# Kernel optimization log

Measured on AMD Instinct MI355X. Metric: run time of the kernel, lower is better.

## Reference

```python
import jax, jax.numpy as jnp
import numpy as np

D_MODEL = 128; D_STATE = 64; HEADDIM = 32; D_CONV = 4; EXPAND = 2
D_INNER = EXPAND * D_MODEL          # 256
NHEADS = D_INNER // HEADDIM         # 8
NGROUPS = 1
D_CONV_CH = D_INNER + 2 * NGROUPS * D_STATE      # 384
D_IN_PROJ = 2 * D_INNER + 2 * NGROUPS * D_STATE + NHEADS  # 648


def _mamba2(u, Win, convw, convb, dtb, Alog, Dp, normw, Wout):
    # u: (B, L, d_model). Mamba2 forward (ngroups=1, rmsnorm gated, no in/out bias).
    B, L, _ = u.shape
    zxbcdt = u @ Win                                   # (B,L,648)
    z, xBC, dt = jnp.split(zxbcdt, [D_INNER, D_INNER + D_CONV_CH], axis=-1)
    # depthwise causal conv1d (kernel D_CONV) + SiLU
    xp = jnp.pad(xBC, ((0, 0), (D_CONV - 1, 0), (0, 0)))
    xconv = sum(xp[:, k:k + L, :] * convw[k] for k in range(D_CONV)) + convb
    xBC = jax.nn.silu(xconv)
    x, Bm, Cm = jnp.split(xBC, [D_INNER, D_INNER + NGROUPS * D_STATE], axis=-1)
    dt = jax.nn.softplus(dt + dtb)                     # (B,L,H)
    A = -jnp.exp(Alog)                                 # (H,)
    xh = x.reshape(B, L, NHEADS, HEADDIM)              # (B,L,H,P)
    dA = jnp.exp(dt * A)                               # (B,L,H)

    def step(h, inp):
        dA_t, dt_t, B_t, C_t, x_t = inp
        h = h * dA_t[:, :, None, None] + jnp.einsum('bh,bn,bhp->bhpn', dt_t, B_t, x_t)
        y = jnp.einsum('bhpn,bn->bhp', h, C_t)
        return h, y

    h0 = jnp.zeros((B, NHEADS, HEADDIM, D_STATE), dtype=u.dtype)
    xs = (jnp.moveaxis(dA, 1, 0), jnp.moveaxis(dt, 1, 0), jnp.moveaxis(Bm, 1, 0),
          jnp.moveaxis(Cm, 1, 0), jnp.moveaxis(xh, 1, 0))
    _, ys = jax.lax.scan(step, h0, xs)
    y = jnp.moveaxis(ys, 0, 1) + Dp[None, None, :, None] * xh   # skip D
    y = y.reshape(B, L, D_INNER)
    # RMSNormGated (norm_before_gate=False): rmsnorm(y * silu(z)) * weight
    y = y * jax.nn.silu(z)
    y = y * jax.lax.rsqrt(jnp.mean(y * y, axis=-1, keepdims=True) + 1e-5) * normw
    return y @ Wout


def _cross_attn(x, ctx, Wq, bq, Wk, bk, Wv, bv, Wo, bo):
    Q = x @ Wq + bq
    K = ctx @ Wk + bk
    V = ctx @ Wv + bv
    att = jax.nn.softmax(jnp.einsum('bqd,bkd->bqk', Q, K) * (D_MODEL ** -0.5), axis=-1)
    return jnp.einsum('bqk,bkd->bqd', att, V) @ Wo + bo


def setup_inputs() -> dict:
    key = jax.random.key(0)
    ks = jax.random.split(key, 8)
    B, L = 2048, 8

    def lin(k, fi, fo):
        return jax.random.normal(k, (fi, fo), jnp.float32) / np.sqrt(fi)

    def mamba_params(kseq):
        k = jax.random.split(kseq, 6)
        dt = jax.random.uniform(k[3], (NHEADS,), minval=0.001, maxval=0.1)
        return {
            'Win': lin(k[0], D_MODEL, D_IN_PROJ),
            'convw': jax.random.normal(k[1], (D_CONV, D_CONV_CH), jnp.float32) * 0.2,
            'convb': jnp.zeros((D_CONV_CH,), jnp.float32),
            'dtb': dt + jnp.log(-jnp.expm1(-dt)),  # inverse softplus
            'Alog': jnp.log(jax.random.uniform(k[4], (NHEADS,), minval=1.0, maxval=16.0)),
            'D': jnp.ones((NHEADS,), jnp.float32),
            'normw': jnp.ones((D_INNER,), jnp.float32),
            'Wout': lin(k[5], D_INNER, D_MODEL),
        }

    inp = {
        'st_feature': jax.random.normal(ks[0], (B, L, D_MODEL), jnp.float32),
        'exp_feature': jax.random.normal(ks[1], (B, L, D_MODEL), jnp.float32),
    }
    for pref, p in (('st_', mamba_params(ks[2])), ('ex_', mamba_params(ks[3]))):
        for n, v in p.items():
            inp[pref + n] = v

    def ca(kseq, pref):
        k = jax.random.split(kseq, 4)
        d = {}
        for n, kk in zip(('Wq', 'Wk', 'Wv', 'Wo'), k):
            d[pref + n] = lin(kk, D_MODEL, D_MODEL)
            d[pref + 'b' + n[1]] = jnp.zeros((D_MODEL,), jnp.float32)
        return d

    inp.update(ca(ks[4], 'cx_'))  # cross_atten_exp
    inp.update(ca(ks[5], 'cs_'))  # cross_atten_st
    inp['mlp_W'] = lin(ks[6], 8 * 2 * D_MODEL, 1024)
    inp['mlp_b'] = jnp.zeros((1024,), jnp.float32)
    return inp


def reference(st_feature, exp_feature,
              st_Win, st_convw, st_convb, st_dtb, st_Alog, st_D, st_normw, st_Wout,
              ex_Win, ex_convw, ex_convb, ex_dtb, ex_Alog, ex_D, ex_normw, ex_Wout,
              cx_Wq, cx_bq, cx_Wk, cx_bk, cx_Wv, cx_bv, cx_Wo, cx_bo,
              cs_Wq, cs_bq, cs_Wk, cs_bk, cs_Wv, cs_bv, cs_Wo, cs_bo,
              mlp_W, mlp_b):
    exp_f = _mamba2(exp_feature, ex_Win, ex_convw, ex_convb, ex_dtb, ex_Alog, ex_D, ex_normw, ex_Wout)
    st_f = _mamba2(st_feature, st_Win, st_convw, st_convb, st_dtb, st_Alog, st_D, st_normw, st_Wout)
    exp_a = _cross_attn(exp_f, st_f, cx_Wq, cx_bq, cx_Wk, cx_bk, cx_Wv, cx_bv, cx_Wo, cx_bo)
    st_a = _cross_attn(st_f, exp_f, cs_Wq, cs_bq, cs_Wk, cs_bk, cs_Wv, cs_bv, cs_Wo, cs_bo)
    x = jnp.concatenate([st_a, exp_a], axis=-1)        # (B, 8, 256)
    x = x.reshape(x.shape[0], -1)                      # (B, 2048)
    return x @ mlp_W + mlp_b
```

## Files before the change

kernel.cpp:

```cpp
#include <hip/hip_runtime.h>
#include <hip/hip_bf16.h>
#include <math.h>

#define B_SZ 2048
#define L_SEQ 8
#define DMODEL 128
#define DSTATE 64
#define HEADDIM 32
#define DCONV 4
#define DINNER 256
#define NHEADS 8
#define DCONVCH 384
#define DINPROJ 648
#define NPAD 656

typedef short bf16x8 __attribute__((ext_vector_type(8)));
typedef float floatx4 __attribute__((ext_vector_type(4)));

__device__ __forceinline__ float siluf(float x) {
    return x / (1.f + expf(-x));
}
__device__ __forceinline__ float bf2f(unsigned short h) {
    unsigned int u = ((unsigned int)h) << 16;
    return __builtin_bit_cast(float, u);
}
__device__ __forceinline__ unsigned short f2bf(float f) {
    __hip_bfloat16 b = __float2bfloat16(f);
    return __builtin_bit_cast(unsigned short, b);
}
__device__ __forceinline__ void unpack8(bf16x8 v, float* o) {
    #pragma unroll
    for (int j = 0; j < 8; ++j) o[j] = bf2f((unsigned short)v[j]);
}
__device__ __forceinline__ void gl_lds16(const unsigned short* g, unsigned short* l) {
    __builtin_amdgcn_global_load_lds(
        (const __attribute__((address_space(1))) unsigned int*)g,
        (__attribute__((address_space(3))) unsigned int*)l, 16, 0, 0);
}

__global__ __launch_bounds__(256) void prep_weights(
    const float* __restrict__ st_Win, const float* __restrict__ ex_Win,
    const float* __restrict__ st_Wout, const float* __restrict__ ex_Wout,
    const float* __restrict__ cs_Wq, const float* __restrict__ cs_Wk,
    const float* __restrict__ cs_Wv, const float* __restrict__ cs_Wo,
    const float* __restrict__ cx_Wq, const float* __restrict__ cx_Wk,
    const float* __restrict__ cx_Wv, const float* __restrict__ cx_Wo,
    const float* __restrict__ mlp_W,
    unsigned short* __restrict__ winT_st, unsigned short* __restrict__ winT_ex,
    unsigned short* __restrict__ woutT_st, unsigned short* __restrict__ woutT_ex,
    unsigned short* __restrict__ attnWT, unsigned short* __restrict__ mlpWt)
{
    __shared__ float tile[32][33];
    int blk = blockIdx.x;
    if (blk < 656) {
        const float* src = blk < 328 ? st_Win : ex_Win;
        unsigned short* dst = blk < 328 ? winT_st : winT_ex;
        int idx = (blk % 328) * 256 + threadIdx.x;
        if (idx >= NPAD * 128) return;
        int n = idx / 128, k = idx % 128;
        float v = (n < DINPROJ) ? src[k * DINPROJ + n] : 0.f;
        dst[idx] = f2bf(v);
    } else if (blk < 912) {
        const float* src = blk < 784 ? st_Wout : ex_Wout;
        unsigned short* dst = blk < 784 ? woutT_st : woutT_ex;
        int idx = ((blk - 656) % 128) * 256 + threadIdx.x;
        int n = idx / 256, k = idx % 256;
        dst[idx] = f2bf(src[k * 128 + n]);
    } else if (blk < 1424) {
        int b2 = blk - 912;
        int mat = b2 >> 6;
        const float* src = mat == 0 ? cs_Wq : mat == 1 ? cs_Wk : mat == 2 ? cs_Wv :
                           mat == 3 ? cs_Wo : mat == 4 ? cx_Wq : mat == 5 ? cx_Wk :
                           mat == 6 ? cx_Wv : cx_Wo;
        int e = (b2 & 63) * 256 + threadIdx.x;
        int n = e >> 7, k = e & 127;
        attnWT[mat * 16384 + n * 128 + k] = f2bf(src[k * 128 + n]);
    } else {
        int b2 = blk - 1424;
        int n0 = (b2 & 31) * 32, k0 = (b2 >> 5) * 32;
        const int tid = threadIdx.x;
        const int c = tid & 31, r0 = tid >> 5;
        for (int rr = r0; rr < 32; rr += 8)
            tile[rr][c] = mlp_W[(size_t)(k0 + rr) * 1024 + n0 + c];
        __syncthreads();
        for (int rr = r0; rr < 32; rr += 8)
            mlpWt[(size_t)(n0 + rr) * 2048 + k0 + c] = f2bf(tile[c][rr]);
    }
}

#define LDK 136
#define LDZ 648
#define LDY 264
__global__ __launch_bounds__(256, 4) void mamba_dual(
    const float* __restrict__ u_ex, const float* __restrict__ u_st,
    const unsigned short* __restrict__ WinT_ex, const unsigned short* __restrict__ WinT_st,
    const float* __restrict__ convw_ex, const float* __restrict__ convw_st,
    const float* __restrict__ convb_ex, const float* __restrict__ convb_st,
    const float* __restrict__ dtb_ex, const float* __restrict__ dtb_st,
    const float* __restrict__ Alog_ex, const float* __restrict__ Alog_st,
    const float* __restrict__ Dp_ex, const float* __restrict__ Dp_st,
    const float* __restrict__ normw_ex, const float* __restrict__ normw_st,
    const unsigned short* __restrict__ WoutT_ex, const unsigned short* __restrict__ WoutT_st,
    unsigned short* __restrict__ out_ex, unsigned short* __restrict__ out_st)
{
    const int which = blockIdx.x >> 10;
    const float* u = which ? u_st : u_ex;
    const unsigned short* WinT = which ? WinT_st : WinT_ex;
    const float* convw = which ? convw_st : convw_ex;
    const float* convb = which ? convb_st : convb_ex;
    const float* dtb = which ? dtb_st : dtb_ex;
    const float* Alog = which ? Alog_st : Alog_ex;
    const float* Dp = which ? Dp_st : Dp_ex;
    const float* normw = which ? normw_st : normw_ex;
    const unsigned short* WoutT = which ? WoutT_st : WoutT_ex;
    unsigned short* outf = which ? out_st : out_ex;

    const int tid = threadIdx.x;
    const int lane = tid & 63;
    const int wave = tid >> 6;
    const int l15 = lane & 15;
    const int q8 = (lane >> 4) * 8;
    const int row0 = (lane >> 4) * 4;
    const int grow0 = (blockIdx.x & 1023) * 16;

    __shared__ __align__(16) unsigned short uA[16 * LDK];
    __shared__ __align__(16) unsigned short zx[16 * LDZ];
    __shared__ __align__(16) unsigned short yb[16 * LDY];
    __shared__ float dtraw[16][8];
    __shared__ float dtv[2][8][8];
    __shared__ float cum[2][8][8];
    __shared__ float Gm[2][8][8];
    __shared__ float red[16][32];
    __shared__ float rstd[16];
    float* coefp = (float*)uA;

    for (int i = tid; i < 512; i += 256) {
        int r = i >> 5, k4 = (i & 31) * 4;
        float4 v = *(const float4*)(u + (size_t)(grow0 + r) * DMODEL + k4);
        ushort4 h;
        h.x = f2bf(v.x); h.y = f2bf(v.y); h.z = f2bf(v.z); h.w = f2bf(v.w);
        *(ushort4*)(uA + r * LDK + k4) = h;
    }
    __syncthreads();

    {
        bf16x8 af[4];
        #pragma unroll
        for (int kk = 0; kk < 4; ++kk)
            af[kk] = *(const bf16x8*)(uA + l15 * LDK + kk * 32 + q8);
        for (int nt = wave; nt < 41; nt += 4) {
            floatx4 acc = {0.f, 0.f, 0.f, 0.f};
            const unsigned short* bp = WinT + (size_t)(nt * 16 + l15) * 128 + q8;
            #pragma unroll
            for (int kk = 0; kk < 4; ++kk) {
                bf16x8 bf = *(const bf16x8*)(bp + kk * 32);
                acc = __builtin_amdgcn_mfma_f32_16x16x32_bf16(af[kk], bf, acc, 0, 0, 0);
            }
            if (nt == 40) {
                if (l15 < 8) {
                    #pragma unroll
                    for (int r = 0; r < 4; ++r)
                        dtraw[row0 + r][l15] = acc[r];
                }
            } else {
                #pragma unroll
                for (int r = 0; r < 4; ++r)
                    zx[(row0 + r) * LDZ + nt * 16 + l15] = f2bf(acc[r]);
            }
        }
    }
    __syncthreads();

    float cv[3][8];
    {
        #pragma unroll
        for (int it = 0; it < 3; ++it) {
            int i = tid + it * 256;
            int r = i / 48, g = i % 48;
            int c0 = g * 8;
            int l = r & 7, bloc = r >> 3;
            float s[8];
            float4 cb0 = *(const float4*)(convb + c0);
            float4 cb1 = *(const float4*)(convb + c0 + 4);
            s[0] = cb0.x; s[1] = cb0.y; s[2] = cb0.z; s[3] = cb0.w;
            s[4] = cb1.x; s[5] = cb1.y; s[6] = cb1.z; s[7] = cb1.w;
            #pragma unroll
            for (int k = 0; k < DCONV; ++k) {
                int lp = l + k - (DCONV - 1);
                if (lp >= 0) {
                    bf16x8 v = *(const bf16x8*)(zx + (bloc * 8 + lp) * LDZ + 256 + c0);
                    float vf[8];
                    unpack8(v, vf);
                    float4 w0 = *(const float4*)(convw + k * DCONVCH + c0);
                    float4 w1 = *(const float4*)(convw + k * DCONVCH + c0 + 4);
                    s[0] += vf[0] * w0.x; s[1] += vf[1] * w0.y;
                    s[2] += vf[2] * w0.z; s[3] += vf[3] * w0.w;
                    s[4] += vf[4] * w1.x; s[5] += vf[5] * w1.y;
                    s[6] += vf[6] * w1.z; s[7] += vf[7] * w1.w;
                }
            }
            #pragma unroll
            for (int j = 0; j < 8; ++j) cv[it][j] = siluf(s[j]);
        }
        if (tid < 128) {
            int r = tid >> 3, h = tid & 7;
            float v = dtraw[r][h] + dtb[h];
            dtv[r >> 3][r & 7][h] = (v > 20.f) ? v : log1pf(expf(v));
        }
    }
    __syncthreads();
    {
        #pragma unroll
        for (int it = 0; it < 3; ++it) {
            int i = tid + it * 256;
            int r = i / 48, c0 = (i % 48) * 8;
            bf16x8 o;
            #pragma unroll
            for (int j = 0; j < 8; ++j) o[j] = (short)f2bf(cv[it][j]);
            *(bf16x8*)(zx + r * LDZ + 256 + c0) = o;
        }
    }
    __syncthreads();

    if (tid < 128) {
        int bloc = tid >> 6, t = (tid >> 3) & 7, s = tid & 7;
        float a = 0.f;
        #pragma unroll
        for (int n = 0; n < DSTATE; n += 8) {
            bf16x8 bv = *(const bf16x8*)(zx + (bloc * 8 + s) * LDZ + 512 + n);
            bf16x8 cvv = *(const bf16x8*)(zx + (bloc * 8 + t) * LDZ + 576 + n);
            float bf_[8], cf_[8];
            unpack8(bv, bf_); unpack8(cvv, cf_);
            #pragma unroll
            for (int j = 0; j < 8; ++j) a += bf_[j] * cf_[j];
        }
        Gm[bloc][t][s] = a;
    } else if (tid < 144) {
        int j = tid - 128;
        int bloc = j >> 3, h = j & 7;
        float c = 0.f;
        for (int l = 0; l < L_SEQ; ++l) { c += dtv[bloc][l][h]; cum[bloc][l][h] = c; }
    }
    __syncthreads();

    for (int i = tid; i < 1024; i += 256) {
        int bloc = i >> 9, t = (i >> 6) & 7, s = (i >> 3) & 7, h = i & 7;
        float A = -expf(Alog[h]);
        coefp[i] = (s <= t)
            ? Gm[bloc][t][s] * expf(A * (cum[bloc][t][h] - cum[bloc][s][h])) * dtv[bloc][s][h]
            : 0.f;
    }
    __syncthreads();

    {
        #pragma unroll
        for (int it = 0; it < 2; ++it) {
            int i = tid + it * 256;
            int r = i >> 5, g = i & 31;
            int c0 = g * 8, h = g >> 2;
            int bloc = r >> 3, t = r & 7;
            float acc[8];
            {
                bf16x8 xv = *(const bf16x8*)(zx + r * LDZ + 256 + c0);
                float xf[8]; unpack8(xv, xf);
                float d = Dp[h];
                #pragma unroll
                for (int j = 0; j < 8; ++j) acc[j] = d * xf[j];
            }
            for (int s = 0; s <= t; ++s) {
                float cf = coefp[((bloc * 8 + t) * 8 + s) * 8 + h];
                bf16x8 xv = *(const bf16x8*)(zx + (bloc * 8 + s) * LDZ + 256 + c0);
                float xf[8]; unpack8(xv, xf);
                #pragma unroll
                for (int j = 0; j < 8; ++j) acc[j] += cf * xf[j];
            }
            bf16x8 zv = *(const bf16x8*)(zx + r * LDZ + c0);
            float zf[8]; unpack8(zv, zf);
            float p = 0.f;
            bf16x8 o;
            #pragma unroll
            for (int j = 0; j < 8; ++j) {
                float y = acc[j] * siluf(zf[j]);
                p += y * y;
                o[j] = (short)f2bf(y);
            }
            *(bf16x8*)(yb + r * LDY + c0) = o;
            red[r][g] = p;
        }
    }
    __syncthreads();
    if (tid < 16) {
        float s = 0.f;
        #pragma unroll
        for (int j = 0; j < 32; ++j) s += red[tid][j];
        rstd[tid] = rsqrtf(s / (float)DINNER + 1e-5f);
    }
    __syncthreads();
    {
        #pragma unroll
        for (int it = 0; it < 2; ++it) {
            int i = tid + it * 256;
            int r = i >> 5, c0 = (i & 31) * 8;
            bf16x8 v = *(const bf16x8*)(yb + r * LDY + c0);
            float vf[8]; unpack8(v, vf);
            float4 w0 = *(const float4*)(normw + c0);
            float4 w1 = *(const float4*)(normw + c0 + 4);
            float rs = rstd[r];
            bf16x8 o;
            o[0] = (short)f2bf(vf[0] * rs * w0.x); o[1] = (short)f2bf(vf[1] * rs * w0.y);
            o[2] = (short)f2bf(vf[2] * rs * w0.z); o[3] = (short)f2bf(vf[3] * rs * w0.w);
            o[4] = (short)f2bf(vf[4] * rs * w1.x); o[5] = (short)f2bf(vf[5] * rs * w1.y);
            o[6] = (short)f2bf(vf[6] * rs * w1.z); o[7] = (short)f2bf(vf[7] * rs * w1.w);
            *(bf16x8*)(yb + r * LDY + c0) = o;
        }
    }
    __syncthreads();

    {
        bf16x8 af[8];
        #pragma unroll
        for (int kk = 0; kk < 8; ++kk)
            af[kk] = *(const bf16x8*)(yb + l15 * LDY + kk * 32 + q8);
        #pragma unroll
        for (int ni = 0; ni < 2; ++ni) {
            int nt = wave * 2 + ni;
            floatx4 acc = {0.f, 0.f, 0.f, 0.f};
            const unsigned short* bp = WoutT + (size_t)(nt * 16 + l15) * 256 + q8;
            #pragma unroll
            for (int kk = 0; kk < 8; ++kk) {
                bf16x8 bf = *(const bf16x8*)(bp + kk * 32);
                acc = __builtin_amdgcn_mfma_f32_16x16x32_bf16(af[kk], bf, acc, 0, 0, 0);
            }
            #pragma unroll
            for (int r = 0; r < 4; ++r)
                outf[(size_t)(grow0 + row0 + r) * DMODEL + nt * 16 + l15] = f2bf(acc[r]);
        }
    }
}

#define ASTR 136
#define VSTR 40
#define PSTR 40
__global__ __launch_bounds__(256, 2) void attn_kernel(
    const unsigned short* __restrict__ st_f,
    const unsigned short* __restrict__ exp_f,
    const unsigned short* __restrict__ WT,
    const float* __restrict__ cs_bq, const float* __restrict__ cs_bk,
    const float* __restrict__ cs_bv, const float* __restrict__ cs_bo,
    const float* __restrict__ cx_bq, const float* __restrict__ cx_bk,
    const float* __restrict__ cx_bv, const float* __restrict__ cx_bo,
    __hip_bfloat16* __restrict__ x)
{
    const int tid = threadIdx.x;
    const int lane = tid & 63, wave = tid >> 6;
    const int l15 = lane & 15;
    const int q8 = (lane >> 4) * 8;
    const int row0 = (lane >> 4) * 4;
    const int grow0 = blockIdx.x * 32;
    const int b0 = blockIdx.x * 4;
    const float scale = 0.08838834764831845f;

    __shared__ __align__(16) unsigned short stf[32 * ASTR];
    __shared__ __align__(16) unsigned short exf[32 * ASTR];
    __shared__ __align__(16) unsigned short Qs[32 * ASTR];
    __shared__ __align__(16) unsigned short Ks[32 * ASTR];
    __shared__ __align__(16) unsigned short attv[32 * ASTR];
    __shared__ __align__(16) unsigned short Vt[128 * VSTR];
    __shared__ __align__(16) unsigned short P[32 * PSTR];
    __shared__ float Ss[32][33];

    #pragma unroll
    for (int it = 0; it < 2; ++it) {
        int i = tid + it * 256;
        int r = i >> 4, c8 = (i & 15) * 8;
        *(uint4*)(stf + r * ASTR + c8) = *(const uint4*)(st_f + (size_t)(grow0 + r) * 128 + c8);
        *(uint4*)(exf + r * ASTR + c8) = *(const uint4*)(exp_f + (size_t)(grow0 + r) * 128 + c8);
    }
    __syncthreads();

    #pragma unroll
    for (int pass = 0; pass < 2; ++pass) {
        const unsigned short* qsrc = pass ? exf : stf;
        const unsigned short* kvsrc = pass ? stf : exf;
        const unsigned short* Wq = WT + (size_t)pass * 4 * 16384;
        const unsigned short* Wk = Wq + 16384;
        const unsigned short* Wv = Wq + 32768;
        const unsigned short* Wo = Wq + 49152;
        const float* bq = pass ? cx_bq : cs_bq;
        const float* bk = pass ? cx_bk : cs_bk;
        const float* bv = pass ? cx_bv : cs_bv;
        const float* bo = pass ? cx_bo : cs_bo;

        {
            bf16x8 aq[2][4], akv[2][4];
            #pragma unroll
            for (int mt = 0; mt < 2; ++mt)
                #pragma unroll
                for (int kk = 0; kk < 4; ++kk) {
                    aq[mt][kk]  = *(const bf16x8*)(qsrc  + (mt * 16 + l15) * ASTR + kk * 32 + q8);
                    akv[mt][kk] = *(const bf16x8*)(kvsrc + (mt * 16 + l15) * ASTR + kk * 32 + q8);
                }
            #pragma unroll
            for (int ni = 0; ni < 2; ++ni) {
                int nc = (wave * 2 + ni) * 16 + l15;
                floatx4 aq0 = {0,0,0,0}, aq1 = {0,0,0,0};
                floatx4 ak0 = {0,0,0,0}, ak1 = {0,0,0,0};
                floatx4 av0 = {0,0,0,0}, av1 = {0,0,0,0};
                #pragma unroll
                for (int kk = 0; kk < 4; ++kk) {
                    bf16x8 wqf = *(const bf16x8*)(Wq + (size_t)nc * 128 + kk * 32 + q8);
                    bf16x8 wkf = *(const bf16x8*)(Wk + (size_t)nc * 128 + kk * 32 + q8);
                    bf16x8 wvf = *(const bf16x8*)(Wv + (size_t)nc * 128 + kk * 32 + q8);
                    aq0 = __builtin_amdgcn_mfma_f32_16x16x32_bf16(aq[0][kk],  wqf, aq0, 0, 0, 0);
                    aq1 = __builtin_amdgcn_mfma_f32_16x16x32_bf16(aq[1][kk],  wqf, aq1, 0, 0, 0);
                    ak0 = __builtin_amdgcn_mfma_f32_16x16x32_bf16(akv[0][kk], wkf, ak0, 0, 0, 0);
                    ak1 = __builtin_amdgcn_mfma_f32_16x16x32_bf16(akv[1][kk], wkf, ak1, 0, 0, 0);
                    av0 = __builtin_amdgcn_mfma_f32_16x16x32_bf16(akv[0][kk], wvf, av0, 0, 0, 0);
                    av1 = __builtin_amdgcn_mfma_f32_16x16x32_bf16(akv[1][kk], wvf, av1, 0, 0, 0);
                }
                float bqv = bq[nc], bkv = bk[nc], bvv = bv[nc];
                #pragma unroll
                for (int r = 0; r < 4; ++r) {
                    Qs[(row0 + r) * ASTR + nc]      = f2bf(aq0[r] + bqv);
                    Qs[(16 + row0 + r) * ASTR + nc] = f2bf(aq1[r] + bqv);
                    Ks[(row0 + r) * ASTR + nc]      = f2bf(ak0[r] + bkv);
                    Ks[(16 + row0 + r) * ASTR + nc] = f2bf(ak1[r] + bkv);
                    Vt[nc * VSTR + row0 + r]        = f2bf(av0[r] + bvv);
                    Vt[nc * VSTR + 16 + row0 + r]   = f2bf(av1[r] + bvv);
                }
            }
        }
        __syncthreads();

        {
            int mtS = wave >> 1, ntS = wave & 1;
            floatx4 s = {0,0,0,0};
            #pragma unroll
            for (int kk = 0; kk < 4; ++kk) {
                bf16x8 a = *(const bf16x8*)(Qs + (mtS * 16 + l15) * ASTR + kk * 32 + q8);
                bf16x8 b = *(const bf16x8*)(Ks + (ntS * 16 + l15) * ASTR + kk * 32 + q8);
                s = __builtin_amdgcn_mfma_f32_16x16x32_bf16(a, b, s, 0, 0, 0);
            }
            #pragma unroll
            for (int r = 0; r < 4; ++r)
                Ss[mtS * 16 + row0 + r][ntS * 16 + l15] = s[r];
        }
        __syncthreads();

        if (tid < 32) {
            int r = tid, c0 = (r >> 3) * 8;
            float v[8], mx = -1e30f;
            #pragma unroll
            for (int c = 0; c < 8; ++c) {
                v[c] = Ss[r][c0 + c] * scale;
                mx = fmaxf(mx, v[c]);
            }
            float sum = 0.f;
            #pragma unroll
            for (int c = 0; c < 8; ++c) { v[c] = expf(v[c] - mx); sum += v[c]; }
            float inv = 1.f / sum;
            #pragma unroll
            for (int c = 0; c < 32; ++c) {
                float pv = (c >= c0 && c < c0 + 8) ? v[c - c0] * inv : 0.f;
                P[r * PSTR + c] = f2bf(pv);
            }
        }
        __syncthreads();

        {
            #pragma unroll
            for (int ni = 0; ni < 2; ++ni) {
                int nc = (wave * 2 + ni) * 16 + l15;
                bf16x8 bv_ = *(const bf16x8*)(Vt + nc * VSTR + q8);
                #pragma unroll
                for (int mt = 0; mt < 2; ++mt) {
                    bf16x8 ap = *(const bf16x8*)(P + (mt * 16 + l15) * PSTR + q8);
                    floatx4 o = {0,0,0,0};
                    o = __builtin_amdgcn_mfma_f32_16x16x32_bf16(ap, bv_, o, 0, 0, 0);
                    #pragma unroll
                    for (int r = 0; r < 4; ++r)
                        attv[(mt * 16 + row0 + r) * ASTR + nc] = f2bf(o[r]);
                }
            }
        }
        __syncthreads();

        {
            bf16x8 ao[2][4];
            #pragma unroll
            for (int mt = 0; mt < 2; ++mt)
                #pragma unroll
                for (int kk = 0; kk < 4; ++kk)
                    ao[mt][kk] = *(const bf16x8*)(attv + (mt * 16 + l15) * ASTR + kk * 32 + q8);
            #pragma unroll
            for (int ni = 0; ni < 2; ++ni) {
                int nc = (wave * 2 + ni) * 16 + l15;
                floatx4 a0 = {0,0,0,0}, a1 = {0,0,0,0};
                #pragma unroll
                for (int kk = 0; kk < 4; ++kk) {
                    bf16x8 wof = *(const bf16x8*)(Wo + (size_t)nc * 128 + kk * 32 + q8);
                    a0 = __builtin_amdgcn_mfma_f32_16x16x32_bf16(ao[0][kk], wof, a0, 0, 0, 0);
                    a1 = __builtin_amdgcn_mfma_f32_16x16x32_bf16(ao[1][kk], wof, a1, 0, 0, 0);
                }
                float bov = bo[nc];
                #pragma unroll
                for (int r = 0; r < 4; ++r) {
                    int rr0 = row0 + r;
                    int rr1 = 16 + row0 + r;
                    x[(size_t)(b0 + (rr0 >> 3)) * 2048 + (rr0 & 7) * 256 + pass * 128 + nc] =
                        __float2bfloat16(a0[r] + bov);
                    x[(size_t)(b0 + (rr1 >> 3)) * 2048 + (rr1 & 7) * 256 + pass * 128 + nc] =
                        __float2bfloat16(a1[r] + bov);
                }
            }
        }
        __syncthreads();
    }
}

__global__ __launch_bounds__(256, 2) void mlp_mfma(
    const unsigned short* __restrict__ X,
    const unsigned short* __restrict__ Wt,
    const float* __restrict__ bias,
    float* __restrict__ out)
{
    __shared__ __align__(16) unsigned short As[64 * 64];
    __shared__ __align__(16) unsigned short Bs[64 * 64];
    const int tid = threadIdx.x;
    const int wave = tid >> 6, lane = tid & 63;
    const int wm = (wave >> 1) * 32, wn = (wave & 1) * 32;
    const int bm = blockIdx.y * 64, bn = blockIdx.x * 64;
    const int l15 = lane & 15, q8 = (lane >> 4) * 8;

    const int c0i = tid, c1i = tid + 256;
    const int r0s = c0i >> 3, c0s = ((c0i & 7) ^ (r0s & 7)) * 8;
    const int r1s = c1i >> 3, c1s = ((c1i & 7) ^ (r1s & 7)) * 8;
    const unsigned short* gA0 = X + (size_t)(bm + r0s) * 2048 + c0s;
    const unsigned short* gA1 = X + (size_t)(bm + r1s) * 2048 + c1s;
    const unsigned short* gB0 = Wt + (size_t)(bn + r0s) * 2048 + c0s;
    const unsigned short* gB1 = Wt + (size_t)(bn + r1s) * 2048 + c1s;
    unsigned short* lA0 = As + c0i * 8;
    unsigned short* lA1 = As + c1i * 8;
    unsigned short* lB0 = Bs + c0i * 8;
    unsigned short* lB1 = Bs + c1i * 8;

    floatx4 acc[2][2];
    #pragma unroll
    for (int i = 0; i < 2; ++i)
        #pragma unroll
        for (int j = 0; j < 2; ++j) acc[i][j] = (floatx4){0.f, 0.f, 0.f, 0.f};

    const int ra0 = wm + l15, ra1 = wm + 16 + l15;
    const int rb0 = wn + l15, rb1 = wn + 16 + l15;

    for (int k0 = 0; k0 < 2048; k0 += 64) {
        __syncthreads();
        gl_lds16(gA0 + k0, lA0);
        gl_lds16(gA1 + k0, lA1);
        gl_lds16(gB0 + k0, lB0);
        gl_lds16(gB1 + k0, lB1);
        __syncthreads();
        #pragma unroll
        for (int ks = 0; ks < 2; ++ks) {
            int xx = ks * 4 + (q8 >> 3);
            bf16x8 a0 = *(const bf16x8*)(As + (ra0 * 8 + (xx ^ (ra0 & 7))) * 8);
            bf16x8 a1 = *(const bf16x8*)(As + (ra1 * 8 + (xx ^ (ra1 & 7))) * 8);
            bf16x8 b0 = *(const bf16x8*)(Bs + (rb0 * 8 + (xx ^ (rb0 & 7))) * 8);
            bf16x8 b1 = *(const bf16x8*)(Bs + (rb1 * 8 + (xx ^ (rb1 & 7))) * 8);
            acc[0][0] = __builtin_amdgcn_mfma_f32_16x16x32_bf16(a0, b0, acc[0][0], 0, 0, 0);
            acc[0][1] = __builtin_amdgcn_mfma_f32_16x16x32_bf16(a0, b1, acc[0][1], 0, 0, 0);
            acc[1][0] = __builtin_amdgcn_mfma_f32_16x16x32_bf16(a1, b0, acc[1][0], 0, 0, 0);
            acc[1][1] = __builtin_amdgcn_mfma_f32_16x16x32_bf16(a1, b1, acc[1][1], 0, 0, 0);
        }
    }

    const int row0 = (lane >> 4) * 4;
    #pragma unroll
    for (int j = 0; j < 2; ++j) {
        int col = bn + wn + j * 16 + l15;
        float bv = bias[col];
        #pragma unroll
        for (int r = 0; r < 4; ++r) {
            out[(size_t)(bm + wm + row0 + r) * 1024 + col] = acc[0][j][r] + bv;
            out[(size_t)(bm + wm + 16 + row0 + r) * 1024 + col] = acc[1][j][r] + bv;
        }
    }
}

extern "C" void kernel_launch(void* const* d_in, const int* in_sizes, int n_in,
                              void* d_out, int out_size, void* d_ws, size_t ws_size,
                              hipStream_t stream) {
    const float* st_feature = (const float*)d_in[0];
    const float* exp_feature = (const float*)d_in[1];
    const float* st_Win = (const float*)d_in[2];
    const float* st_convw = (const float*)d_in[3];
    const float* st_convb = (const float*)d_in[4];
    const float* st_dtb = (const float*)d_in[5];
    const float* st_Alog = (const float*)d_in[6];
    const float* st_D = (const float*)d_in[7];
    const float* st_normw = (const float*)d_in[8];
    const float* st_Wout = (const float*)d_in[9];
    const float* ex_Win = (const float*)d_in[10];
    const float* ex_convw = (const float*)d_in[11];
    const float* ex_convb = (const float*)d_in[12];
    const float* ex_dtb = (const float*)d_in[13];
    const float* ex_Alog = (const float*)d_in[14];
    const float* ex_D = (const float*)d_in[15];
    const float* ex_normw = (const float*)d_in[16];
    const float* ex_Wout = (const float*)d_in[17];
    const float* cx_Wq = (const float*)d_in[18]; const float* cx_bq = (const float*)d_in[19];
    const float* cx_Wk = (const float*)d_in[20]; const float* cx_bk = (const float*)d_in[21];
    const float* cx_Wv = (const float*)d_in[22]; const float* cx_bv = (const float*)d_in[23];
    const float* cx_Wo = (const float*)d_in[24]; const float* cx_bo = (const float*)d_in[25];
    const float* cs_Wq = (const float*)d_in[26]; const float* cs_bq = (const float*)d_in[27];
    const float* cs_Wk = (const float*)d_in[28]; const float* cs_bk = (const float*)d_in[29];
    const float* cs_Wv = (const float*)d_in[30]; const float* cs_bv = (const float*)d_in[31];
    const float* cs_Wo = (const float*)d_in[32]; const float* cs_bo = (const float*)d_in[33];
    const float* mlp_W = (const float*)d_in[34];
    const float* mlp_b = (const float*)d_in[35];

    unsigned short* wsu = (unsigned short*)d_ws;
    unsigned short* st_fb  = wsu;
    unsigned short* exp_fb = st_fb + (size_t)B_SZ * L_SEQ * DMODEL;
    unsigned short* xbuf   = exp_fb + (size_t)B_SZ * L_SEQ * DMODEL;
    unsigned short* wtbuf  = xbuf + (size_t)2048 * 2048;
    unsigned short* winT_st = wtbuf + (size_t)1024 * 2048;
    unsigned short* winT_ex = winT_st + (size_t)NPAD * 128;
    unsigned short* woutT_st = winT_ex + (size_t)NPAD * 128;
    unsigned short* woutT_ex = woutT_st + (size_t)128 * 256;
    unsigned short* attnWT  = woutT_ex + (size_t)128 * 256;

    prep_weights<<<3472, 256, 0, stream>>>(
        st_Win, ex_Win, st_Wout, ex_Wout,
        cs_Wq, cs_Wk, cs_Wv, cs_Wo, cx_Wq, cx_Wk, cx_Wv, cx_Wo, mlp_W,
        winT_st, winT_ex, woutT_st, woutT_ex, attnWT, wtbuf);
    mamba_dual<<<2048, 256, 0, stream>>>(
        exp_feature, st_feature, winT_ex, winT_st,
        ex_convw, st_convw, ex_convb, st_convb,
        ex_dtb, st_dtb, ex_Alog, st_Alog, ex_D, st_D,
        ex_normw, st_normw, woutT_ex, woutT_st,
        exp_fb, st_fb);
    attn_kernel<<<B_SZ / 4, 256, 0, stream>>>(st_fb, exp_fb, attnWT,
                                              cs_bq, cs_bk, cs_bv, cs_bo,
                                              cx_bq, cx_bk, cx_bv, cx_bo,
                                              (__hip_bfloat16*)xbuf);
    {
        dim3 g(1024 / 64, 2048 / 64);
        mlp_mfma<<<g, 256, 0, stream>>>(xbuf, wtbuf, mlp_b, (float*)d_out);
    }
}
```

Before: 253.5 us.

## Cut mamba LDS usage for occupancy and enlarge MLP GEMM tile to 128x64

The mamba kernel drops its separate y buffer and reduction array. It keeps gated y values in registers, computes the RMS sum with wave shuffles, and writes the normalized output into the reused zx buffer. This lets launch bounds rise to 5 blocks per CU. The MLP GEMM tile grows from 64x64 to 128x64 with 4x2 MFMA accumulators per wave, which improves A/B reuse and halves the grid. The tradeoffs are higher register pressure and fewer blocks in the MLP, and reusing zx as ybA assumes zx is no longer read when it is overwritten.

```diff
diff --git a/kernel.cpp b/kernel.cpp
--- a/kernel.cpp
+++ b/kernel.cpp
@@ -91,7 +91,7 @@
 #define LDK 136
 #define LDZ 648
 #define LDY 264
-__global__ __launch_bounds__(256, 4) void mamba_dual(
+__global__ __launch_bounds__(256, 5) void mamba_dual(
     const float* __restrict__ u_ex, const float* __restrict__ u_st,
     const unsigned short* __restrict__ WinT_ex, const unsigned short* __restrict__ WinT_st,
     const float* __restrict__ convw_ex, const float* __restrict__ convw_st,
@@ -125,14 +125,13 @@
 
     __shared__ __align__(16) unsigned short uA[16 * LDK];
     __shared__ __align__(16) unsigned short zx[16 * LDZ];
-    __shared__ __align__(16) unsigned short yb[16 * LDY];
     __shared__ float dtraw[16][8];
     __shared__ float dtv[2][8][8];
     __shared__ float cum[2][8][8];
     __shared__ float Gm[2][8][8];
-    __shared__ float red[16][32];
     __shared__ float rstd[16];
     float* coefp = (float*)uA;
+    unsigned short* ybA = zx;
 
     for (int i = tid; i < 512; i += 256) {
         int r = i >> 5, k4 = (i & 31) * 4;
@@ -252,7 +251,9 @@
     }
     __syncthreads();
 
+    float yv[2][8];
     {
+        float psum[2];
         #pragma unroll
         for (int it = 0; it < 2; ++it) {
             int i = tid + it * 256;
@@ -277,41 +278,45 @@
             bf16x8 zv = *(const bf16x8*)(zx + r * LDZ + c0);
             float zf[8]; unpack8(zv, zf);
             float p = 0.f;
-            bf16x8 o;
             #pragma unroll
             for (int j = 0; j < 8; ++j) {
                 float y = acc[j] * siluf(zf[j]);
                 p += y * y;
-                o[j] = (short)f2bf(y);
-            }
-            *(bf16x8*)(yb + r * LDY + c0) = o;
-            red[r][g] = p;
-        }
-    }
-    __syncthreads();
-    if (tid < 16) {
-        float s = 0.f;
-        #pragma unroll
-        for (int j = 0; j < 32; ++j) s += red[tid][j];
-        rstd[tid] = rsqrtf(s / (float)DINNER + 1e-5f);
-    }
-    __syncthreads();
+                yv[it][j] = y;
+            }
+            psum[it] = p;
+        }
+        #pragma unroll
+        for (int off = 16; off > 0; off >>= 1) {
+            psum[0] += __shfl_down(psum[0], off, 32);
+            psum[1] += __shfl_down(psum[1], off, 32);
+        }
+        if ((lane & 31) == 0) {
+            int r = tid >> 5;
+            rstd[r]     = rsqrtf(psum[0] * (1.f / DINNER) + 1e-5f);
+            rstd[r + 8] = rsqrtf(psum[1] * (1.f / DINNER) + 1e-5f);
+        }
+    }
+    __syncthreads();
+
     {
         #pragma unroll
         for (int it = 0; it < 2; ++it) {
             int i = tid + it * 256;
             int r = i >> 5, c0 = (i & 31) * 8;
-            bf16x8 v = *(const bf16x8*)(yb + r * LDY + c0);
-            float vf[8]; unpack8(v, vf);
+            float rs = rstd[r];
             float4 w0 = *(const float4*)(normw + c0);
             float4 w1 = *(const float4*)(normw + c0 + 4);
-            float rs = rstd[r];
             bf16x8 o;
-            o[0] = (short)f2bf(vf[0] * rs * w0.x); o[1] = (short)f2bf(vf[1] * rs * w0.y);
-            o[2] = (short)f2bf(vf[2] * rs * w0.z); o[3] = (short)f2bf(vf[3] * rs * w0.w);
-            o[4] = (short)f2bf(vf[4] * rs * w1.x); o[5] = (short)f2bf(vf[5] * rs * w1.y);
-            o[6] = (short)f2bf(vf[6] * rs * w1.z); o[7] = (short)f2bf(vf[7] * rs * w1.w);
-            *(bf16x8*)(yb + r * LDY + c0) = o;
+            o[0] = (short)f2bf(yv[it][0] * rs * w0.x);
+            o[1] = (short)f2bf(yv[it][1] * rs * w0.y);
+            o[2] = (short)f2bf(yv[it][2] * rs * w0.z);
+            o[3] = (short)f2bf(yv[it][3] * rs * w0.w);
+            o[4] = (short)f2bf(yv[it][4] * rs * w1.x);
+            o[5] = (short)f2bf(yv[it][5] * rs * w1.y);
+            o[6] = (short)f2bf(yv[it][6] * rs * w1.z);
+            o[7] = (short)f2bf(yv[it][7] * rs * w1.w);
+            *(bf16x8*)(ybA + r * LDY + c0) = o;
         }
     }
     __syncthreads();
@@ -320,7 +325,7 @@
         bf16x8 af[8];
         #pragma unroll
         for (int kk = 0; kk < 8; ++kk)
-            af[kk] = *(const bf16x8*)(yb + l15 * LDY + kk * 32 + q8);
+            af[kk] = *(const bf16x8*)(ybA + l15 * LDY + kk * 32 + q8);
         #pragma unroll
         for (int ni = 0; ni < 2; ++ni) {
             int nt = wave * 2 + ni;
@@ -518,71 +523,80 @@
     }
 }
 
-__global__ __launch_bounds__(256, 2) void mlp_mfma(
+__global__ __launch_bounds__(256) void mlp_mfma(
     const unsigned short* __restrict__ X,
     const unsigned short* __restrict__ Wt,
     const float* __restrict__ bias,
     float* __restrict__ out)
 {
-    __shared__ __align__(16) unsigned short As[64 * 64];
+    __shared__ __align__(16) unsigned short As[128 * 64];
     __shared__ __align__(16) unsigned short Bs[64 * 64];
     const int tid = threadIdx.x;
     const int wave = tid >> 6, lane = tid & 63;
-    const int wm = (wave >> 1) * 32, wn = (wave & 1) * 32;
-    const int bm = blockIdx.y * 64, bn = blockIdx.x * 64;
+    const int wm = (wave >> 1) * 64, wn = (wave & 1) * 32;
+    const int bm = blockIdx.y * 128, bn = blockIdx.x * 64;
     const int l15 = lane & 15, q8 = (lane >> 4) * 8;
 
-    const int c0i = tid, c1i = tid + 256;
-    const int r0s = c0i >> 3, c0s = ((c0i & 7) ^ (r0s & 7)) * 8;
-    const int r1s = c1i >> 3, c1s = ((c1i & 7) ^ (r1s & 7)) * 8;
-    const unsigned short* gA0 = X + (size_t)(bm + r0s) * 2048 + c0s;
-    const unsigned short* gA1 = X + (size_t)(bm + r1s) * 2048 + c1s;
-    const unsigned short* gB0 = Wt + (size_t)(bn + r0s) * 2048 + c0s;
-    const unsigned short* gB1 = Wt + (size_t)(bn + r1s) * 2048 + c1s;
-    unsigned short* lA0 = As + c0i * 8;
-    unsigned short* lA1 = As + c1i * 8;
-    unsigned short* lB0 = Bs + c0i * 8;
-    unsigned short* lB1 = Bs + c1i * 8;
-
-    floatx4 acc[2][2];
+    const unsigned short* gA[4];
+    const unsigned short* gB[2];
     #pragma unroll
-    for (int i = 0; i < 2; ++i)
+    for (int j = 0; j < 4; ++j) {
+        int cid = tid + j * 256;
+        int r = cid >> 3, c16 = ((cid & 7) ^ (r & 7)) * 8;
+        gA[j] = X + (size_t)(bm + r) * 2048 + c16;
+    }
+    #pragma unroll
+    for (int j = 0; j < 2; ++j) {
+        int cid = tid + j * 256;
+        int r = cid >> 3, c16 = ((cid & 7) ^ (r & 7)) * 8;
+        gB[j] = Wt + (size_t)(bn + r) * 2048 + c16;
+    }
+
+    floatx4 acc[4][2];
+    #pragma unroll
+    for (int i = 0; i < 4; ++i)
         #pragma unroll
         for (int j = 0; j < 2; ++j) acc[i][j] = (floatx4){0.f, 0.f, 0.f, 0.f};
 
-    const int ra0 = wm + l15, ra1 = wm + 16 + l15;
-    const int rb0 = wn + l15, rb1 = wn + 16 + l15;
-
     for (int k0 = 0; k0 < 2048; k0 += 64) {
         __syncthreads();
-        gl_lds16(gA0 + k0, lA0);
-        gl_lds16(gA1 + k0, lA1);
-        gl_lds16(gB0 + k0, lB0);
-        gl_lds16(gB1 + k0, lB1);
+        #pragma unroll
+        for (int j = 0; j < 4; ++j) gl_lds16(gA[j] + k0, As + (tid + j * 256) * 8);
+        #pragma unroll
+        for (int j = 0; j < 2; ++j) gl_lds16(gB[j] + k0, Bs + (tid + j * 256) * 8);
         __syncthreads();
         #pragma unroll
         for (int ks = 0; ks < 2; ++ks) {
             int xx = ks * 4 + (q8 >> 3);
-            bf16x8 a0 = *(const bf16x8*)(As + (ra0 * 8 + (xx ^ (ra0 & 7))) * 8);
-            bf16x8 a1 = *(const bf16x8*)(As + (ra1 * 8 + (xx ^ (ra1 & 7))) * 8);
-            bf16x8 b0 = *(const bf16x8*)(Bs + (rb0 * 8 + (xx ^ (rb0 & 7))) * 8);
-            bf16x8 b1 = *(const bf16x8*)(Bs + (rb1 * 8 + (xx ^ (rb1 & 7))) * 8);
-            acc[0][0] = __builtin_amdgcn_mfma_f32_16x16x32_bf16(a0, b0, acc[0][0], 0, 0, 0);
-            acc[0][1] = __builtin_amdgcn_mfma_f32_16x16x32_bf16(a0, b1, acc[0][1], 0, 0, 0);
-            acc[1][0] = __builtin_amdgcn_mfma_f32_16x16x32_bf16(a1, b0, acc[1][0], 0, 0, 0);
-            acc[1][1] = __builtin_amdgcn_mfma_f32_16x16x32_bf16(a1, b1, acc[1][1], 0, 0, 0);
+            bf16x8 a[4], b[2];
+            #pragma unroll
+            for (int mi = 0; mi < 4; ++mi) {
+                int ra = wm + mi * 16 + l15;
+                a[mi] = *(const bf16x8*)(As + (ra * 8 + (xx ^ (ra & 7))) * 8);
+            }
+            #pragma unroll
+            for (int ni = 0; ni < 2; ++ni) {
+                int rb = wn + ni * 16 + l15;
+                b[ni] = *(const bf16x8*)(Bs + (rb * 8 + (xx ^ (rb & 7))) * 8);
+            }
+            #pragma unroll
+            for (int mi = 0; mi < 4; ++mi)
+                #pragma unroll
+                for (int ni = 0; ni < 2; ++ni)
+                    acc[mi][ni] = __builtin_amdgcn_mfma_f32_16x16x32_bf16(a[mi], b[ni], acc[mi][ni], 0, 0, 0);
         }
     }
 
     const int row0 = (lane >> 4) * 4;
     #pragma unroll
-    for (int j = 0; j < 2; ++j) {
-        int col = bn + wn + j * 16 + l15;
+    for (int ni = 0; ni < 2; ++ni) {
+        int col = bn + wn + ni * 16 + l15;
         float bv = bias[col];
         #pragma unroll
-        for (int r = 0; r < 4; ++r) {
-            out[(size_t)(bm + wm + row0 + r) * 1024 + col] = acc[0][j][r] + bv;
-            out[(size_t)(bm + wm + 16 + row0 + r) * 1024 + col] = acc[1][j][r] + bv;
+        for (int mi = 0; mi < 4; ++mi) {
+            #pragma unroll
+            for (int r = 0; r < 4; ++r)
+                out[(size_t)(bm + wm + mi * 16 + row0 + r) * 1024 + col] = acc[mi][ni][r] + bv;
         }
     }
 }
@@ -645,7 +659,7 @@
                                               cx_bq, cx_bk, cx_bv, cx_bo,
                                               (__hip_bfloat16*)xbuf);
     {
-        dim3 g(1024 / 64, 2048 / 64);
+        dim3 g(1024 / 64, 2048 / 128);
         mlp_mfma<<<g, 256, 0, stream>>>(xbuf, wtbuf, mlp_b, (float*)d_out);
     }
 }
```

New measurement: 263.5 us. +3.9%, slower.
